# Performance work log

Hardware: AMD Instinct MI355X
Metric: run time of the kernel (lower is better)

The kernel has to match this reference:

```python
import jax, jax.numpy as jnp
import numpy as np

FP8_MAX = 448.0  # max normal of float8_e4m3fn
NUM_HEADS = 16


def act_quant(x):
    # per-tensor fp8 quantization: scale so max|x| maps to FP8_MAX
    scale = jnp.max(jnp.abs(x)) / FP8_MAX
    q = (x / scale).astype(jnp.float8_e4m3fn)
    return q, scale


def setup_inputs() -> dict:
    key = jax.random.key(0)
    k1, k2, k3, k4 = jax.random.split(key, 4)
    B, S, H = 2, 2048, 2048
    x = jax.random.normal(k1, (B, S, H), dtype=jnp.float32)
    W_qkv = jax.random.normal(k2, (H, 3 * H), dtype=jnp.float32) * (1.0 / np.sqrt(H))
    W_out = jax.random.normal(k3, (H, H), dtype=jnp.float32) * (1.0 / np.sqrt(H))
    b_out = jnp.zeros((H,), dtype=jnp.float32)
    return {"x": x, "W_qkv": W_qkv, "W_out": W_out, "b_out": b_out}


def reference(x, W_qkv, W_out, b_out):
    B, S, H = x.shape
    nH = NUM_HEADS
    hd = H // nH  # 128, matches head_dim default used for scaling

    qkv = jnp.einsum('bsh,hf->bsf', x, W_qkv)          # [B,S,3H]
    qkv = qkv.reshape(B, S, 3, nH, hd)
    q = qkv[:, :, 0].transpose(0, 2, 1, 3)             # [B,nH,S,hd]
    k = qkv[:, :, 1].transpose(0, 2, 1, 3)
    v = qkv[:, :, 2].transpose(0, 2, 1, 3)

    q8, q_scale = act_quant(q)
    k8, k_scale = act_quant(k)
    # fp8_gemm_optimized: dequantized GEMM = (a @ b) * a_scale * b_scale
    scores = jnp.einsum('bhqd,bhkd->bhqk',
                        q8.astype(jnp.float32), k8.astype(jnp.float32))
    scores = scores * (q_scale * k_scale) / jnp.sqrt(jnp.float32(hd))

    attn = jax.nn.softmax(scores, axis=-1)             # [B,nH,S,S]
    # (dropout omitted: deterministic / eval mode)

    v8, v_scale = act_quant(v)
    out = jnp.einsum('bhqk,bhkd->bhqd', attn, v8.astype(jnp.float32))
    out = out * v_scale                                # a_scale = 1 for attn weights

    out = out.transpose(0, 2, 1, 3).reshape(B, S, H)
    return jnp.einsum('bsh,ho->bso', out, W_out) + b_out
```

## Files before the change

kernel.cpp:

```cpp
#include <hip/hip_runtime.h>
#include <hip/hip_bf16.h>
#include <math.h>

#define B_   2
#define S_   2048
#define H_   2048
#define NH   16
#define HD   128
#define ROWS (B_ * S_)
#define F3   (3 * H_)
#define KS   2048

typedef _Float16 f16x8 __attribute__((ext_vector_type(8)));
typedef float    f32x4  __attribute__((ext_vector_type(4)));
typedef float    f32x16 __attribute__((ext_vector_type(16)));

union H2 { unsigned u; _Float16 h[2]; };
union H4 { ushort4 s4; _Float16 h[4]; };
union H4b { uint2 u2; _Float16 h[4]; };
union PU { unsigned u[4]; f16x8 v8; };

__device__ __forceinline__ void gl_lds16(const void* g, void* l) {
  __builtin_amdgcn_global_load_lds(
      (const __attribute__((address_space(1))) void*)g,
      (__attribute__((address_space(3))) void*)l, 16, 0, 0);
}

__device__ __forceinline__ float quant_e4m3(float x) {
  float ax = fabsf(x);
  float q;
  if (ax < 0.015625f) {
    q = rintf(ax * 512.0f) * (1.0f / 512.0f);
  } else {
    unsigned eb = __float_as_uint(ax) & 0x7f800000u;
    float quantum = __uint_as_float(eb - (3u << 23));
    q = rintf(ax / quantum) * quantum;
    if (q > 448.0f) q = 448.0f;
  }
  return copysignf(q, x);
}

__global__ __launch_bounds__(256) void prep_split(
    const float* __restrict__ x, const float* __restrict__ Wqkv,
    _Float16* __restrict__ A1hi, _Float16* __restrict__ A1lo,
    _Float16* __restrict__ B1thi, _Float16* __restrict__ B1tlo) {
  __shared__ _Float16 ht[64][72];
  __shared__ _Float16 lt[64][72];
  const int t = threadIdx.x;
  const int bid = blockIdx.x;
  if (bid < 8192) {
    const size_t i = (size_t)bid * 256 + t;
    float4 v = ((const float4*)x)[i];
    H4 h, l;
    h.h[0] = (_Float16)v.x; l.h[0] = (_Float16)(v.x - (float)h.h[0]);
    h.h[1] = (_Float16)v.y; l.h[1] = (_Float16)(v.y - (float)h.h[1]);
    h.h[2] = (_Float16)v.z; l.h[2] = (_Float16)(v.z - (float)h.h[2]);
    h.h[3] = (_Float16)v.w; l.h[3] = (_Float16)(v.w - (float)h.h[3]);
    ((ushort4*)A1hi)[i] = h.s4;
    ((ushort4*)A1lo)[i] = l.s4;
  } else {
    const int idx = bid - 8192;
    const int n0 = (idx % 96) * 64, k0 = (idx / 96) * 64;
    const int K = H_, N = F3;
#pragma unroll
    for (int p = 0; p < 4; p++) {
      const int k = p * 16 + (t >> 4);
      const int n = (t & 15) * 4;
      float4 v = *(const float4*)(Wqkv + (size_t)(k0 + k) * N + n0 + n);
      _Float16 h0 = (_Float16)v.x, h1 = (_Float16)v.y,
               h2 = (_Float16)v.z, h3 = (_Float16)v.w;
      ht[n + 0][k] = h0; lt[n + 0][k] = (_Float16)(v.x - (float)h0);
      ht[n + 1][k] = h1; lt[n + 1][k] = (_Float16)(v.y - (float)h1);
      ht[n + 2][k] = h2; lt[n + 2][k] = (_Float16)(v.z - (float)h2);
      ht[n + 3][k] = h3; lt[n + 3][k] = (_Float16)(v.w - (float)h3);
    }
    __syncthreads();
#pragma unroll
    for (int it = 0; it < 2; it++) {
      const int idx2 = it * 256 + t;
      const int r = idx2 >> 3, c = (idx2 & 7) * 8;
      *(uint4*)(B1thi + (size_t)(n0 + r) * K + k0 + c) = *(const uint4*)&ht[r][c];
      *(uint4*)(B1tlo + (size_t)(n0 + r) * K + k0 + c) = *(const uint4*)&lt[r][c];
    }
  }
}

__global__ __launch_bounds__(256) void split_tr(
    const float* __restrict__ in, _Float16* __restrict__ hi,
    _Float16* __restrict__ lo, int K, int N) {
  __shared__ _Float16 ht[64][72];
  __shared__ _Float16 lt[64][72];
  const int t = threadIdx.x;
  const int n0 = blockIdx.x * 64, k0 = blockIdx.y * 64;
#pragma unroll
  for (int p = 0; p < 4; p++) {
    const int k = p * 16 + (t >> 4);
    const int n = (t & 15) * 4;
    float4 v = *(const float4*)(in + (size_t)(k0 + k) * N + n0 + n);
    _Float16 h0 = (_Float16)v.x, h1 = (_Float16)v.y,
             h2 = (_Float16)v.z, h3 = (_Float16)v.w;
    ht[n + 0][k] = h0; lt[n + 0][k] = (_Float16)(v.x - (float)h0);
    ht[n + 1][k] = h1; lt[n + 1][k] = (_Float16)(v.y - (float)h1);
    ht[n + 2][k] = h2; lt[n + 2][k] = (_Float16)(v.z - (float)h2);
    ht[n + 3][k] = h3; lt[n + 3][k] = (_Float16)(v.w - (float)h3);
  }
  __syncthreads();
#pragma unroll
  for (int it = 0; it < 2; it++) {
    const int idx = it * 256 + t;
    const int r = idx >> 3, c = (idx & 7) * 8;
    *(uint4*)(hi + (size_t)(n0 + r) * K + k0 + c) = *(const uint4*)&ht[r][c];
    *(uint4*)(lo + (size_t)(n0 + r) * K + k0 + c) = *(const uint4*)&lt[r][c];
  }
}

#define STAGE_A(tt, dst) do {                                                  \
    const _Float16* As_ = ((tt) < 64) ? Ahi : Alo;                             \
    const size_t so_ = (size_t)(row0 + wave * 8 + srow) * KS +                 \
                       (((tt) & 31) << 6) + schunk;                            \
    _Float16* db_ = (dst) + wave * 512;                                        \
    gl_lds16(As_ + so_,                    db_);                               \
    gl_lds16(As_ + so_ + (size_t)64 * KS,  db_ + 4096);                        \
    gl_lds16(As_ + so_ + (size_t)128 * KS, db_ + 8192);                       \
    gl_lds16(As_ + so_ + (size_t)192 * KS, db_ + 12288);                       \
  } while (0)

#define STAGE_B(tt, dst) do {                                                  \
    const _Float16* Bs_ = ((((tt) >> 5)) == 1) ? Btlo : Bthi;                  \
    const size_t so_ = (size_t)(col0 + wave * 8 + srow) * KS +                 \
                       (((tt) & 31) << 6) + schunk;                            \
    _Float16* db_ = (dst) + 16384 + wave * 512;                                \
    gl_lds16(Bs_ + so_,                    db_);                               \
    gl_lds16(Bs_ + so_ + (size_t)64 * KS,  db_ + 4096);                        \
  } while (0)

__global__ __launch_bounds__(512, 2) void gemm_split256(
    const _Float16* __restrict__ Ahi, const _Float16* __restrict__ Alo,
    const _Float16* __restrict__ Bthi, const _Float16* __restrict__ Btlo,
    float* __restrict__ C, const float* __restrict__ bias,
    unsigned* mx, int N, int has_bias) {
  __shared__ __align__(16) _Float16 lds[73728];
  const int t = threadIdx.x;
  const int wave = t >> 6, lane = t & 63;
  const int l15 = lane & 15, g = lane >> 4;
  const int wm = wave >> 1, wn = wave & 1;

  const int gx = gridDim.x;
  const int nwg = gx * gridDim.y;
  const int bid = blockIdx.y * gx + blockIdx.x;
  const int tile = (bid & 7) * (nwg >> 3) + (bid >> 3);
  const int row0 = (tile / gx) * 256, col0 = (tile % gx) * 128;

  const int srow = lane >> 3;
  const int schunk = ((lane & 7) ^ srow) << 3;

  f32x4 acc[4][4] = {};

  _Float16* bufA = lds;
  _Float16* bufB = lds + 24576;
  _Float16* bufC = lds + 49152;

  STAGE_A(0, bufA);
  STAGE_B(0, bufA);
  STAGE_A(1, bufB);
  STAGE_B(1, bufB);
  asm volatile("s_waitcnt vmcnt(6)" ::: "memory");
  __builtin_amdgcn_s_barrier();

  for (int kc = 0; kc < 96; kc++) {
    const _Float16* Ab = bufA;
    const _Float16* Bb = bufA + 16384;
    f16x8 af0[4], bf0[4], af1[4], bf1[4];
#pragma unroll
    for (int i = 0; i < 4; i++) {
      const int r_ = wm * 64 + i * 16 + l15;
      af0[i] = *(const f16x8*)(Ab + r_ * 64 + ((g ^ (r_ & 7)) << 3));
      af1[i] = *(const f16x8*)(Ab + r_ * 64 + (((4 ^ g) ^ (r_ & 7)) << 3));
    }
#pragma unroll
    for (int j = 0; j < 4; j++) {
      const int r_ = wn * 64 + j * 16 + l15;
      bf0[j] = *(const f16x8*)(Bb + r_ * 64 + ((g ^ (r_ & 7)) << 3));
      bf1[j] = *(const f16x8*)(Bb + r_ * 64 + (((4 ^ g) ^ (r_ & 7)) << 3));
    }
    if (kc + 2 < 96) {
      STAGE_A(kc + 2, bufC);
      STAGE_B(kc + 2, bufC);
    }
#pragma unroll
    for (int i = 0; i < 4; i++)
#pragma unroll
      for (int j = 0; j < 4; j++)
        acc[i][j] = __builtin_amdgcn_mfma_f32_16x16x32_f16(af0[i], bf0[j], acc[i][j], 0, 0, 0);
#pragma unroll
    for (int i = 0; i < 4; i++)
#pragma unroll
      for (int j = 0; j < 4; j++)
        acc[i][j] = __builtin_amdgcn_mfma_f32_16x16x32_f16(af1[i], bf1[j], acc[i][j], 0, 0, 0);
    if (kc < 94) { asm volatile("s_waitcnt vmcnt(6)" ::: "memory"); }
    else         { asm volatile("s_waitcnt vmcnt(0)" ::: "memory"); }
    __builtin_amdgcn_s_barrier();
    _Float16* tmp = bufA; bufA = bufB; bufB = bufC; bufC = tmp;
  }

  float bmax = 0.0f;
#pragma unroll
  for (int j = 0; j < 4; j++) {
    const int col = col0 + wn * 64 + j * 16 + l15;
    const float bv = has_bias ? bias[col] : 0.0f;
#pragma unroll
    for (int i = 0; i < 4; i++) {
      const int rbase = row0 + wm * 64 + i * 16 + g * 4;
#pragma unroll
      for (int r = 0; r < 4; r++) {
        const float v = acc[i][j][r] + bv;
        C[(size_t)(rbase + r) * N + col] = v;
        bmax = fmaxf(bmax, fabsf(v));
      }
    }
  }

  if (mx) {
    __syncthreads();
    float* red = (float*)lds;
    red[t] = bmax;
    __syncthreads();
    for (int s2 = 256; s2 > 0; s2 >>= 1) {
      if (t < s2) red[t] = fmaxf(red[t], red[t + s2]);
      __syncthreads();
    }
    if (t == 0) atomicMax(mx + (col0 >> 11), __float_as_uint(red[0]));
  }
}

__global__ __launch_bounds__(256) void quant_qkv(
    const float* __restrict__ qkv, const unsigned* __restrict__ mx,
    _Float16* __restrict__ q8, _Float16* __restrict__ k8,
    _Float16* __restrict__ v8t) {
  __shared__ _Float16 tile[64 * 72];
  const int t = threadIdx.x;
  const int bid = blockIdx.x;

  if (bid < 16384) {
    const size_t base = ((size_t)bid * 256 + t) * 4;
    const int row = (int)(base >> 12);
    const int col = (int)(base & 4095);
    const int seg = col >> 11;
    const int c2 = col & 2047;
    const int h = c2 >> 7, d = c2 & 127;
    const int b = row >> 11, s = row & 2047;
    const float scale = __uint_as_float(mx[seg]) / 448.0f;
    float4 v = *(const float4*)(qkv + (size_t)row * F3 + col);
    H4 r;
    r.h[0] = (_Float16)quant_e4m3(v.x / scale);
    r.h[1] = (_Float16)quant_e4m3(v.y / scale);
    r.h[2] = (_Float16)quant_e4m3(v.z / scale);
    r.h[3] = (_Float16)quant_e4m3(v.w / scale);
    _Float16* dst = seg ? k8 : q8;
    const size_t di = ((size_t)((b * NH + h) * S_) + s) * HD + d;
    *(ushort4*)(dst + di) = r.s4;
  } else {
    const int bt = bid - 16384;
    const int dtile = bt & 1;
    const int stile = (bt >> 1) & 31;
    const int bh = bt >> 6;
    const int b = bh >> 4, h = bh & 15;
    const int s0 = stile * 64, d0 = dtile * 64;
    const float scale = __uint_as_float(mx[2]) / 448.0f;

#pragma unroll
    for (int r = 0; r < 4; r++) {
      const int s = s0 + r * 16 + (t >> 4);
      const int dl = (t & 15) * 4;
      float4 v = *(const float4*)(qkv + (size_t)(b * S_ + s) * F3 + 4096 + h * HD + d0 + dl);
      tile[(dl + 0) * 72 + r * 16 + (t >> 4)] = (_Float16)quant_e4m3(v.x / scale);
      tile[(dl + 1) * 72 + r * 16 + (t >> 4)] = (_Float16)quant_e4m3(v.y / scale);
      tile[(dl + 2) * 72 + r * 16 + (t >> 4)] = (_Float16)quant_e4m3(v.z / scale);
      tile[(dl + 3) * 72 + r * 16 + (t >> 4)] = (_Float16)quant_e4m3(v.w / scale);
    }
    __syncthreads();
#pragma unroll
    for (int j = 0; j < 2; j++) {
      const int wi = j * 256 + t;
      const int dl = wi >> 3;
      const int sch = (wi & 7) * 8;
      uint4 val = *(const uint4*)(tile + dl * 72 + sch);
      *(uint4*)(v8t + (size_t)bh * (HD * S_) + (size_t)(d0 + dl) * S_ + s0 + sch) = val;
    }
  }
}

__global__ __launch_bounds__(256, 2) void attn_kernel(
    const _Float16* __restrict__ q8, const _Float16* __restrict__ k8,
    const _Float16* __restrict__ v8t, const unsigned* __restrict__ mx,
    _Float16* __restrict__ oHi, _Float16* __restrict__ oLo) {
  __shared__ __align__(16) char ldsb[65536];

  const int t = threadIdx.x;
  const int wave = t >> 6;
  const int lane = t & 63;
  const int l31 = lane & 31;
  const int hf = lane >> 5;

  const int qt = blockIdx.x & 15;
  const int bh = blockIdx.x >> 4;
  const int b = bh >> 4, h = bh & 15;
  const int q0 = qt * 128 + wave * 32;

  const float qs = __uint_as_float(mx[0]) * (1.0f / 448.0f);
  const float ks = __uint_as_float(mx[1]) * (1.0f / 448.0f);
  const float vs = __uint_as_float(mx[2]) * (1.0f / 448.0f);
  const float sfac = qs * ks * 0.08838834764831843f;

  f16x8 qf[8];
  {
    const _Float16* qp = q8 + ((size_t)(bh * S_) + q0 + l31) * HD + hf * 8;
#pragma unroll
    for (int st = 0; st < 8; st++)
      qf[st] = *(const f16x8*)(qp + st * 16);
  }

  f32x16 acc[4] = {};
  float m_base = 0.0f;
  float l_run = 0.0f;

  const size_t kB_ = (size_t)(bh * S_) * HD;
  const size_t vB_ = (size_t)bh * (HD * S_);
  const int k_key = t >> 4;
  const int k_dch = (t & 15) * 8;
  const int k_wch = (((t & 15) ^ (k_key & 7)) << 3);
  const int v_d   = t >> 3;
  const int v_sch = (t & 7) * 8;
  const int v_wch = (((t & 7) ^ (v_d & 7)) << 3);

  const int NT = S_ / 64;
  uint4 kp[4], vp[4];

#pragma unroll
  for (int r = 0; r < 4; r++)
    kp[r] = *(const uint4*)(k8 + kB_ + (size_t)(r * 16 + k_key) * HD + k_dch);
#pragma unroll
  for (int r = 0; r < 4; r++)
    vp[r] = *(const uint4*)(v8t + vB_ + (size_t)(r * 32 + v_d) * S_ + v_sch);
  {
    _Float16* K0 = (_Float16*)ldsb;
    _Float16* V0 = (_Float16*)(ldsb + 32768);
#pragma unroll
    for (int r = 0; r < 4; r++)
      *(uint4*)(K0 + (r * 16 + k_key) * 128 + k_wch) = kp[r];
#pragma unroll
    for (int r = 0; r < 4; r++)
      *(uint4*)(V0 + (r * 32 + v_d) * 64 + v_wch) = vp[r];
  }
#pragma unroll
  for (int r = 0; r < 4; r++)
    kp[r] = *(const uint4*)(k8 + kB_ + (size_t)(64 + r * 16 + k_key) * HD + k_dch);
#pragma unroll
  for (int r = 0; r < 4; r++)
    vp[r] = *(const uint4*)(v8t + vB_ + (size_t)(r * 32 + v_d) * S_ + 64 + v_sch);
  __syncthreads();

  for (int kt = 0; kt < NT; kt++) {
    const _Float16* Klds  = (const _Float16*)(ldsb + (kt & 1) * 16384);
    const _Float16* VTlds = (const _Float16*)(ldsb + 32768 + (kt & 1) * 16384);
    if (kt + 1 < NT) {
      _Float16* Kn = (_Float16*)(ldsb + ((kt + 1) & 1) * 16384);
      _Float16* Vn = (_Float16*)(ldsb + 32768 + ((kt + 1) & 1) * 16384);
#pragma unroll
      for (int r = 0; r < 4; r++)
        *(uint4*)(Kn + (r * 16 + k_key) * 128 + k_wch) = kp[r];
#pragma unroll
      for (int r = 0; r < 4; r++)
        *(uint4*)(Vn + (r * 32 + v_d) * 64 + v_wch) = vp[r];
    }
    if (kt + 2 < NT) {
      const int nk = (kt + 2) * 64;
#pragma unroll
      for (int r = 0; r < 4; r++)
        kp[r] = *(const uint4*)(k8 + kB_ + (size_t)(nk + r * 16 + k_key) * HD + k_dch);
#pragma unroll
      for (int r = 0; r < 4; r++)
        vp[r] = *(const uint4*)(v8t + vB_ + (size_t)(r * 32 + v_d) * S_ + nk + v_sch);
    }

    f32x16 s0 = {}, s1 = {};
    __builtin_amdgcn_s_setprio(1);
#pragma unroll
    for (int st = 0; st < 8; st++) {
      const int kr0 = l31;
      const int kr1 = 32 + l31;
      f16x8 a0 = *(const f16x8*)(Klds + kr0 * 128 +
                                 (((st * 2 + hf) ^ (kr0 & 7)) << 3));
      f16x8 a1 = *(const f16x8*)(Klds + kr1 * 128 +
                                 (((st * 2 + hf) ^ (kr1 & 7)) << 3));
      s0 = __builtin_amdgcn_mfma_f32_32x32x16_f16(a0, qf[st], s0, 0, 0, 0);
      s1 = __builtin_amdgcn_mfma_f32_32x32x16_f16(a1, qf[st], s1, 0, 0, 0);
    }
    __builtin_amdgcn_s_setprio(0);

    f16x8 vf00 = *(const f16x8*)(VTlds + l31 * 64 + (((0 + hf) ^ (l31 & 7)) << 3));
    f16x8 vf01 = *(const f16x8*)(VTlds + l31 * 64 + (((2 + hf) ^ (l31 & 7)) << 3));
    f16x8 vf10 = *(const f16x8*)(VTlds + l31 * 64 + (((4 + hf) ^ (l31 & 7)) << 3));
    f16x8 vf11 = *(const f16x8*)(VTlds + l31 * 64 + (((6 + hf) ^ (l31 & 7)) << 3));

    float p0[16], p1[16];
    if (kt == 0) {
      float tmax = -3.0e38f;
#pragma unroll
      for (int i = 0; i < 16; i++) {
        p0[i] = s0[i] * sfac;
        tmax = fmaxf(tmax, p0[i]);
      }
      tmax = fmaxf(tmax, __shfl_xor(tmax, 32));
      m_base = tmax;
      float rs = 0.0f;
#pragma unroll
      for (int i = 0; i < 16; i++) {
        p0[i] = __expf(p0[i] - tmax);
        rs += p0[i];
      }
      l_run += rs;
    } else {
      const float mb = m_base;
      float rs = 0.0f;
#pragma unroll
      for (int i = 0; i < 16; i++) {
        p0[i] = fminf(__expf(fmaf(s0[i], sfac, -mb)), 60000.0f);
        rs += p0[i];
      }
      l_run += rs;
    }
    {
      const float mb = m_base;
      float rs = 0.0f;
#pragma unroll
      for (int i = 0; i < 16; i++) {
        p1[i] = fminf(__expf(fmaf(s1[i], sfac, -mb)), 60000.0f);
        rs += p1[i];
      }
      l_run += rs;
    }

    f16x8 pf0[2], pf1[2];
#pragma unroll
    for (int sb = 0; sb < 2; sb++) {
      const float* pp = sb ? p1 : p0;
      f16x8* pf = sb ? pf1 : pf0;
#pragma unroll
      for (int c = 0; c < 2; c++) {
        const int c8 = c * 8;
        const int sidx = hf ? 0 : 4;
        const int oidx = hf ? 4 : 0;
        H2 s0h, s1h, o0h, o1h;
        s0h.h[0] = (_Float16)pp[c8 + sidx];     s0h.h[1] = (_Float16)pp[c8 + sidx + 1];
        s1h.h[0] = (_Float16)pp[c8 + sidx + 2]; s1h.h[1] = (_Float16)pp[c8 + sidx + 3];
        o0h.h[0] = (_Float16)pp[c8 + oidx];     o0h.h[1] = (_Float16)pp[c8 + oidx + 1];
        o1h.h[0] = (_Float16)pp[c8 + oidx + 2]; o1h.h[1] = (_Float16)pp[c8 + oidx + 3];
        unsigned r0 = (unsigned)__shfl_xor((int)s0h.u, 32);
        unsigned r1 = (unsigned)__shfl_xor((int)s1h.u, 32);
        PU pu;
        if (hf == 0) { pu.u[0] = o0h.u; pu.u[1] = o1h.u; pu.u[2] = r0; pu.u[3] = r1; }
        else         { pu.u[0] = r0;    pu.u[1] = r1;    pu.u[2] = o0h.u; pu.u[3] = o1h.u; }
        pf[c] = pu.v8;
      }
    }

#pragma unroll
    for (int dt = 0; dt < 4; dt++) {
      f16x8 n00, n01, n10, n11;
      if (dt < 3) {
        const int vrow = (dt + 1) * 32 + l31;
        n00 = *(const f16x8*)(VTlds + vrow * 64 + (((0 + hf) ^ (vrow & 7)) << 3));
        n01 = *(const f16x8*)(VTlds + vrow * 64 + (((2 + hf) ^ (vrow & 7)) << 3));
        n10 = *(const f16x8*)(VTlds + vrow * 64 + (((4 + hf) ^ (vrow & 7)) << 3));
        n11 = *(const f16x8*)(VTlds + vrow * 64 + (((6 + hf) ^ (vrow & 7)) << 3));
      }
      __builtin_amdgcn_s_setprio(1);
      acc[dt] = __builtin_amdgcn_mfma_f32_32x32x16_f16(vf00, pf0[0], acc[dt], 0, 0, 0);
      acc[dt] = __builtin_amdgcn_mfma_f32_32x32x16_f16(vf01, pf0[1], acc[dt], 0, 0, 0);
      acc[dt] = __builtin_amdgcn_mfma_f32_32x32x16_f16(vf10, pf1[0], acc[dt], 0, 0, 0);
      acc[dt] = __builtin_amdgcn_mfma_f32_32x32x16_f16(vf11, pf1[1], acc[dt], 0, 0, 0);
      __builtin_amdgcn_s_setprio(0);
      vf00 = n00; vf01 = n01; vf10 = n10; vf11 = n11;
    }
    __syncthreads();
  }

  l_run += __shfl_xor(l_run, 32);
  const float f = vs / l_run;

  _Float16* obuf = (_Float16*)ldsb;
  const int obase = wave * 4352;
#pragma unroll
  for (int pass = 0; pass < 2; pass++) {
    __syncthreads();
#pragma unroll
    for (int dt = 0; dt < 4; dt++) {
#pragma unroll
      for (int iq = 0; iq < 4; iq++) {
        const int dl0 = 8 * iq + 4 * hf;
        H4b w;
#pragma unroll
        for (int e = 0; e < 4; e++) {
          const float o = acc[dt][iq * 4 + e] * f;
          const _Float16 hh = (_Float16)o;
          w.h[e] = pass ? (_Float16)(o - (float)hh) : hh;
        }
        *(uint2*)&obuf[obase + l31 * 136 + dt * 32 + dl0] = w.u2;
      }
    }
    __syncthreads();
    _Float16* dst = pass ? oLo : oHi;
#pragma unroll
    for (int ii = 0; ii < 8; ii++) {
      const int qrow = ii * 4 + (lane >> 4);
      const int ch = (lane & 15) * 8;
      uint4 val = *(const uint4*)&obuf[obase + qrow * 136 + ch];
      const size_t ofs = (size_t)(b * S_ + q0 + qrow) * H_ + h * HD + ch;
      *(uint4*)(dst + ofs) = val;
    }
  }
}

extern "C" void kernel_launch(void* const* d_in, const int* in_sizes, int n_in,
                              void* d_out, int out_size, void* d_ws, size_t ws_size,
                              hipStream_t stream) {
  const float* x     = (const float*)d_in[0];
  const float* W_qkv = (const float*)d_in[1];
  const float* W_out = (const float*)d_in[2];
  const float* b_out = (const float*)d_in[3];
  float* out = (float*)d_out;

  char* ws = (char*)d_ws;
  float*    qkv    = (float*)ws;
  _Float16* A2hi   = (_Float16*)(ws + 33554432);
  _Float16* A2lo   = (_Float16*)(ws + 50331648);
  _Float16* B2thi  = (_Float16*)(ws + 67108864);
  _Float16* B2tlo  = (_Float16*)(ws + 75497472);
  _Float16* B1thi  = (_Float16*)(ws + 100663296);
  _Float16* B1tlo  = (_Float16*)(ws + 125829120);
  _Float16* q8     = (_Float16*)(ws + 100663296);
  _Float16* k8     = (_Float16*)(ws + 117440512);
  _Float16* v8t    = (_Float16*)(ws + 134217728);
  _Float16* A1hi   = (_Float16*)(ws + 150994944);
  _Float16* A1lo   = (_Float16*)(ws + 167772160);
  unsigned* mx     = (unsigned*)(ws + 184549376);

  hipMemsetAsync(mx, 0, 3 * sizeof(unsigned), stream);

  prep_split<<<11264, 256, 0, stream>>>(x, W_qkv, A1hi, A1lo, B1thi, B1tlo);

  gemm_split256<<<dim3(F3 / 128, ROWS / 256), 512, 0, stream>>>(
      A1hi, A1lo, B1thi, B1tlo, qkv, nullptr, mx, F3, 0);

  quant_qkv<<<16384 + B_ * NH * 32 * 2, 256, 0, stream>>>(qkv, mx, q8, k8, v8t);

  attn_kernel<<<B_ * NH * 16, 256, 0, stream>>>(q8, k8, v8t, mx, A2hi, A2lo);

  split_tr<<<dim3(H_ / 64, H_ / 64), 256, 0, stream>>>(W_out, B2thi, B2tlo, H_, H_);

  gemm_split256<<<dim3(H_ / 128, ROWS / 256), 512, 0, stream>>>(
      A2hi, A2lo, B2thi, B2tlo, out, b_out, nullptr, H_, 1);
}
```

Measured before the change: 718.3 us.

## Software-pipeline QK^T one tile ahead of softmax and PV in attention loop

Computes the score tile for key block kt+1 before doing the softmax and PV MFMAs for block kt. The goal is to let the MFMA work of the next QK^T overlap with the exp/convert VALU work of the current tile, hiding dependency stalls. It adds a second __syncthreads per iteration so the freshly written next K buffer is visible before it is read. It also holds two extra 16-float accumulators live, which raises register pressure and may cut occupancy.

Measured after the change: 699.7 us. -2.6%, faster.

```diff
diff --git a/kernel.cpp b/kernel.cpp
--- a/kernel.cpp
+++ b/kernel.cpp
@@ -360,9 +360,22 @@
     vp[r] = *(const uint4*)(v8t + vB_ + (size_t)(r * 32 + v_d) * S_ + 64 + v_sch);
   __syncthreads();
 
+  f32x16 sc0 = {}, sc1 = {};
+  {
+    const _Float16* K0 = (const _Float16*)ldsb;
+    __builtin_amdgcn_s_setprio(1);
+#pragma unroll
+    for (int st = 0; st < 8; st++) {
+      const int kr0 = l31, kr1 = 32 + l31;
+      f16x8 a0 = *(const f16x8*)(K0 + kr0 * 128 + (((st * 2 + hf) ^ (kr0 & 7)) << 3));
+      f16x8 a1 = *(const f16x8*)(K0 + kr1 * 128 + (((st * 2 + hf) ^ (kr1 & 7)) << 3));
+      sc0 = __builtin_amdgcn_mfma_f32_32x32x16_f16(a0, qf[st], sc0, 0, 0, 0);
+      sc1 = __builtin_amdgcn_mfma_f32_32x32x16_f16(a1, qf[st], sc1, 0, 0, 0);
+    }
+    __builtin_amdgcn_s_setprio(0);
+  }
+
   for (int kt = 0; kt < NT; kt++) {
-    const _Float16* Klds  = (const _Float16*)(ldsb + (kt & 1) * 16384);
-    const _Float16* VTlds = (const _Float16*)(ldsb + 32768 + (kt & 1) * 16384);
     if (kt + 1 < NT) {
       _Float16* Kn = (_Float16*)(ldsb + ((kt + 1) & 1) * 16384);
       _Float16* Vn = (_Float16*)(ldsb + 32768 + ((kt + 1) & 1) * 16384);
@@ -382,22 +395,24 @@
       for (int r = 0; r < 4; r++)
         vp[r] = *(const uint4*)(v8t + vB_ + (size_t)(r * 32 + v_d) * S_ + nk + v_sch);
     }
-
-    f32x16 s0 = {}, s1 = {};
-    __builtin_amdgcn_s_setprio(1);
-#pragma unroll
-    for (int st = 0; st < 8; st++) {
-      const int kr0 = l31;
-      const int kr1 = 32 + l31;
-      f16x8 a0 = *(const f16x8*)(Klds + kr0 * 128 +
-                                 (((st * 2 + hf) ^ (kr0 & 7)) << 3));
-      f16x8 a1 = *(const f16x8*)(Klds + kr1 * 128 +
-                                 (((st * 2 + hf) ^ (kr1 & 7)) << 3));
-      s0 = __builtin_amdgcn_mfma_f32_32x32x16_f16(a0, qf[st], s0, 0, 0, 0);
-      s1 = __builtin_amdgcn_mfma_f32_32x32x16_f16(a1, qf[st], s1, 0, 0, 0);
-    }
-    __builtin_amdgcn_s_setprio(0);
-
+    __syncthreads();
+
+    f32x16 sn0 = {}, sn1 = {};
+    if (kt + 1 < NT) {
+      const _Float16* Kn = (const _Float16*)(ldsb + ((kt + 1) & 1) * 16384);
+      __builtin_amdgcn_s_setprio(1);
+#pragma unroll
+      for (int st = 0; st < 8; st++) {
+        const int kr0 = l31, kr1 = 32 + l31;
+        f16x8 a0 = *(const f16x8*)(Kn + kr0 * 128 + (((st * 2 + hf) ^ (kr0 & 7)) << 3));
+        f16x8 a1 = *(const f16x8*)(Kn + kr1 * 128 + (((st * 2 + hf) ^ (kr1 & 7)) << 3));
+        sn0 = __builtin_amdgcn_mfma_f32_32x32x16_f16(a0, qf[st], sn0, 0, 0, 0);
+        sn1 = __builtin_amdgcn_mfma_f32_32x32x16_f16(a1, qf[st], sn1, 0, 0, 0);
+      }
+      __builtin_amdgcn_s_setprio(0);
+    }
+
+    const _Float16* VTlds = (const _Float16*)(ldsb + 32768 + (kt & 1) * 16384);
     f16x8 vf00 = *(const f16x8*)(VTlds + l31 * 64 + (((0 + hf) ^ (l31 & 7)) << 3));
     f16x8 vf01 = *(const f16x8*)(VTlds + l31 * 64 + (((2 + hf) ^ (l31 & 7)) << 3));
     f16x8 vf10 = *(const f16x8*)(VTlds + l31 * 64 + (((4 + hf) ^ (l31 & 7)) << 3));
@@ -408,7 +423,7 @@
       float tmax = -3.0e38f;
 #pragma unroll
       for (int i = 0; i < 16; i++) {
-        p0[i] = s0[i] * sfac;
+        p0[i] = sc0[i] * sfac;
         tmax = fmaxf(tmax, p0[i]);
       }
       tmax = fmaxf(tmax, __shfl_xor(tmax, 32));
@@ -425,7 +440,7 @@
       float rs = 0.0f;
 #pragma unroll
       for (int i = 0; i < 16; i++) {
-        p0[i] = fminf(__expf(fmaf(s0[i], sfac, -mb)), 60000.0f);
+        p0[i] = fminf(__expf(fmaf(sc0[i], sfac, -mb)), 60000.0f);
         rs += p0[i];
       }
       l_run += rs;
@@ -435,7 +450,7 @@
       float rs = 0.0f;
 #pragma unroll
       for (int i = 0; i < 16; i++) {
-        p1[i] = fminf(__expf(fmaf(s1[i], sfac, -mb)), 60000.0f);
+        p1[i] = fminf(__expf(fmaf(sc1[i], sfac, -mb)), 60000.0f);
         rs += p1[i];
       }
       l_run += rs;
@@ -484,6 +499,7 @@
       vf00 = n00; vf01 = n01; vf10 = n10; vf11 = n11;
     }
     __syncthreads();
+    sc0 = sn0; sc1 = sn1;
   }
 
   l_run += __shfl_xor(l_run, 32);
```
